# Performance work log

Hardware: AMD Instinct MI355X
Metric: run time of the kernel (lower is better)

Reference implementation:

```python
import jax, jax.numpy as jnp
import numpy as np
from jax import lax

B, NPG = 128, 1024          # graphs, nodes per graph
N = B * NPG                  # total nodes
AVG_DEG = 8
E = N * AVG_DEG              # total edges
F_N, F_E = 128, 32           # node / edge feature dims
LATENT = [32, 32, 32, 1]
D = sum(LATENT)              # total_latent_dim = 97
K = 30                       # sort-pooling k
C1, C2, KW2 = 16, 32, 5      # conv1d channels / kernel
OUT = 2
DENSE = ((K - 2) // 2 + 1 - KW2 + 1) * C2  # 352


def setup_inputs() -> dict:
    key = jax.random.key(0)
    ks = jax.random.split(key, 12)
    inp = {}
    inp["node_feat"] = jax.random.normal(ks[0], (N, F_N), jnp.float32)
    inp["edge_feat"] = jax.random.normal(ks[1], (E, F_E), jnp.float32)
    inp["edge_index"] = jax.random.randint(ks[2], (2, E), 0, N)
    dims = [F_N + F_E] + LATENT
    for i in range(4):
        inp[f"W{i}"] = jax.random.normal(ks[3 + i], (dims[i], dims[i + 1]), jnp.float32) * 0.05
        inp[f"b{i}"] = jnp.zeros((dims[i + 1],), jnp.float32)
    inp["w_conv1"] = jax.random.normal(ks[7], (C1, 1, D), jnp.float32) * 0.05
    inp["b_conv1"] = jnp.zeros((C1,), jnp.float32)
    inp["w_conv2"] = jax.random.normal(ks[8], (C2, C1, KW2), jnp.float32) * 0.05
    inp["b_conv2"] = jnp.zeros((C2,), jnp.float32)
    inp["w_out"] = jax.random.normal(ks[9], (DENSE, OUT), jnp.float32) * 0.05
    inp["b_out"] = jnp.zeros((OUT,), jnp.float32)
    return inp


def _maxpool2(x):
    # MaxPool1d(2, 2) over last axis of [B, C, L]
    return lax.reduce_window(x, -jnp.inf, lax.max, (1, 1, 2), (1, 1, 2), "VALID")


def _forward(node_feat, edge_feat, W0, b0, W1, b1, W2, b2, W3, b3,
             w_conv1, b_conv1, w_conv2, b_conv2, w_out, b_out, edge_index):
    src, dst = edge_index[0], edge_index[1]
    # degree with self-loop, as in DGCNN (divide by deg after linear)
    deg = jnp.ones((N,), node_feat.dtype).at[dst].add(1.0)
    # e2npool: sum incident edge features onto destination nodes
    e2n = jax.ops.segment_sum(edge_feat, dst, num_segments=N)
    cur = jnp.concatenate([node_feat, e2n], axis=1)  # [N, F_N+F_E]
    hops = []
    for W, b in ((W0, b0), (W1, b1), (W2, b2), (W3, b3)):
        # (A + I) X  -> Linear -> / deg -> tanh
        pooled = jax.ops.segment_sum(cur[src], dst, num_segments=N) + cur
        cur = jnp.tanh((pooled @ W + b) / deg[:, None])
        hops.append(cur)
    feat = jnp.concatenate(hops, axis=1).reshape(B, NPG, D)  # [B, NPG, 97]
    # SortPooling: top-k nodes per graph by last latent channel
    _, idx = lax.top_k(feat[:, :, -1], K)                    # [B, K]
    sp = jnp.take_along_axis(feat, idx[:, :, None], axis=1)  # [B, K, D]
    x = sp.reshape(B, 1, K * D)
    x = lax.conv_general_dilated(x, w_conv1, (D,), "VALID",
                                 dimension_numbers=("NCH", "OIH", "NCH"))
    x = jax.nn.relu(x + b_conv1[None, :, None])  # [B, 16, 30]
    x = _maxpool2(x)                              # [B, 16, 15]
    x = lax.conv_general_dilated(x, w_conv2, (1,), "VALID",
                                 dimension_numbers=("NCH", "OIH", "NCH"))
    x = jax.nn.relu(x + b_conv2[None, :, None])  # [B, 32, 11]
    x = x.reshape(B, -1)                          # [B, 352]
    return jax.nn.relu(x @ w_out + b_out)         # [B, OUT]


def reference(node_feat, edge_feat, edge_index, W0, b0, W1, b1, W2, b2, W3, b3,
              w_conv1, b_conv1, w_conv2, b_conv2, w_out, b_out):
    return _forward(node_feat, edge_feat, W0, b0, W1, b1, W2, b2, W3, b3,
                    w_conv1, b_conv1, w_conv2, b_conv2, w_out, b_out, edge_index)
```

## Files before the change

kernel.cpp:

```cpp
#include <hip/hip_runtime.h>
#include <hip/hip_bf16.h>
#include <math.h>

#define N_NODES 131072
#define N_EDGES 1048576
#define B_GR    128
#define NPG_    1024
#define KTOP    30


__global__ __launch_bounds__(256) void k_zero(int* cnt) {
    int i = blockIdx.x * 256 + threadIdx.x;
    if (i < N_NODES) cnt[i] = 0;
}

__global__ __launch_bounds__(256) void k_count(const int* __restrict__ dst, int* __restrict__ cnt) {
    int e = blockIdx.x * 256 + threadIdx.x;
    if (e < N_EDGES) atomicAdd(&cnt[dst[e]], 1);
}

__global__ __launch_bounds__(256) void k_scan1(const int* __restrict__ cnt,
                                               int* __restrict__ row_start,
                                               int* __restrict__ blocksum) {
    __shared__ int s[256];
    int t = threadIdx.x;
    int i = blockIdx.x * 256 + t;
    int v = cnt[i];
    s[t] = v; __syncthreads();
    for (int o = 1; o < 256; o <<= 1) {
        int x = (t >= o) ? s[t - o] : 0;
        __syncthreads();
        s[t] += x;
        __syncthreads();
    }
    row_start[i] = s[t] - v;
    if (t == 255) blocksum[blockIdx.x] = s[t];
}

__global__ __launch_bounds__(512) void k_scan2(int* __restrict__ blocksum) {
    __shared__ int s[512];
    int t = threadIdx.x;
    int v = blocksum[t];
    s[t] = v; __syncthreads();
    for (int o = 1; o < 512; o <<= 1) {
        int x = (t >= o) ? s[t - o] : 0;
        __syncthreads();
        s[t] += x;
        __syncthreads();
    }
    blocksum[t] = s[t] - v;
}

__global__ __launch_bounds__(256) void k_scan3(int* __restrict__ row_start,
                                               const int* __restrict__ blocksum,
                                               int* __restrict__ cursor) {
    int i = blockIdx.x * 256 + threadIdx.x;
    int r = row_start[i] + blocksum[blockIdx.x];
    row_start[i] = r;
    cursor[i] = r;
}

__global__ __launch_bounds__(256) void k_fill(const int* __restrict__ src,
                                              const int* __restrict__ dst,
                                              int* __restrict__ cursor,
                                              int2* __restrict__ csr) {
    int e = blockIdx.x * 256 + threadIdx.x;
    if (e < N_EDGES) {
        int d = dst[e];
        int pos = atomicAdd(&cursor[d], 1);
        csr[pos] = make_int2(src[e], e);
    }
}


__global__ __launch_bounds__(256) void k_esum(const float* __restrict__ ef,
                                              const int* __restrict__ row_start,
                                              const int* __restrict__ cnt,
                                              const int2* __restrict__ csr,
                                              float* __restrict__ esum) {
    int g = threadIdx.x >> 5, j = threadIdx.x & 31;
    int n = blockIdx.x * 8 + g;
    int start = row_start[n], len = cnt[n];
    const int2* ce = csr + start;
    float s = 0.f;
    int i = 0;
    for (; i + 8 <= len; i += 8) {
        int e0 = ce[i].y, e1 = ce[i + 1].y, e2 = ce[i + 2].y, e3 = ce[i + 3].y;
        int e4 = ce[i + 4].y, e5 = ce[i + 5].y, e6 = ce[i + 6].y, e7 = ce[i + 7].y;
        float a0 = ef[(size_t)e0 * 32 + j], a1 = ef[(size_t)e1 * 32 + j];
        float a2 = ef[(size_t)e2 * 32 + j], a3 = ef[(size_t)e3 * 32 + j];
        float a4 = ef[(size_t)e4 * 32 + j], a5 = ef[(size_t)e5 * 32 + j];
        float a6 = ef[(size_t)e6 * 32 + j], a7 = ef[(size_t)e7 * 32 + j];
        s += ((a0 + a1) + (a2 + a3)) + ((a4 + a5) + (a6 + a7));
    }
    for (; i < len; ++i) s += ef[(size_t)ce[i].y * 32 + j];
    esum[(size_t)n * 32 + j] = s;
}


__global__ __launch_bounds__(256) void k_gemm160(const float* __restrict__ nf,
                                                 const float* __restrict__ esum,
                                                 const float* __restrict__ W0,
                                                 float* __restrict__ z0) {
    __shared__ float a[64 * 161];
    int tid = threadIdx.x;
    int n0 = blockIdx.x * 64;
    const float* nfb = nf + (size_t)n0 * 128;
    for (int f = tid; f < 8192; f += 256) {
        int n = f >> 7, k = f & 127;
        a[n * 161 + k] = nfb[f];
    }
    const float* esb = esum + (size_t)n0 * 32;
    for (int f = tid; f < 2048; f += 256) {
        int n = f >> 5, k = f & 31;
        a[n * 161 + 128 + k] = esb[f];
    }
    __syncthreads();
    int wv = __builtin_amdgcn_readfirstlane(tid >> 6);
    int lane = tid & 63;
    int c0 = wv * 8;
    float acc[8] = {0.f, 0.f, 0.f, 0.f, 0.f, 0.f, 0.f, 0.f};
    const float* ar = a + lane * 161;
    for (int k = 0; k < 160; ++k) {
        float av = ar[k];
        #pragma unroll
        for (int jj = 0; jj < 8; ++jj)
            acc[jj] += av * W0[k * 32 + c0 + jj];
    }
    float* zr = z0 + (size_t)(n0 + lane) * 32 + c0;
    *(float4*)zr = make_float4(acc[0], acc[1], acc[2], acc[3]);
    *(float4*)(zr + 4) = make_float4(acc[4], acc[5], acc[6], acc[7]);
}


__global__ __launch_bounds__(256) void k_gemm32(const float* __restrict__ h,
                                                const float* __restrict__ W,
                                                float* __restrict__ zout) {
    __shared__ float a[64 * 33];
    int tid = threadIdx.x;
    int n0 = blockIdx.x * 64;
    const float* hb = h + (size_t)n0 * 32;
    for (int f = tid; f < 2048; f += 256) {
        int n = f >> 5, k = f & 31;
        a[n * 33 + k] = hb[f];
    }
    __syncthreads();
    int wv = __builtin_amdgcn_readfirstlane(tid >> 6);
    int lane = tid & 63;
    int c0 = wv * 8;
    float acc[8] = {0.f, 0.f, 0.f, 0.f, 0.f, 0.f, 0.f, 0.f};
    const float* ar = a + lane * 33;
    #pragma unroll
    for (int k = 0; k < 32; ++k) {
        float av = ar[k];
        #pragma unroll
        for (int jj = 0; jj < 8; ++jj)
            acc[jj] += av * W[k * 32 + c0 + jj];
    }
    float* zr = zout + (size_t)(n0 + lane) * 32 + c0;
    *(float4*)zr = make_float4(acc[0], acc[1], acc[2], acc[3]);
    *(float4*)(zr + 4) = make_float4(acc[4], acc[5], acc[6], acc[7]);
}


__global__ __launch_bounds__(256) void k_g(const float* __restrict__ zin,
                                           const int* __restrict__ row_start,
                                           const int* __restrict__ cnt,
                                           const int2* __restrict__ csr,
                                           const float* __restrict__ bias,
                                           float* __restrict__ hout) {
    int g = threadIdx.x >> 5, j = threadIdx.x & 31;
    int n = blockIdx.x * 8 + g;
    int start = row_start[n], len = cnt[n];
    const int2* cs = csr + start;
    float p = zin[(size_t)n * 32 + j];
    int i = 0;
    for (; i + 8 <= len; i += 8) {
        int s0 = cs[i].x, s1 = cs[i + 1].x, s2 = cs[i + 2].x, s3 = cs[i + 3].x;
        int s4 = cs[i + 4].x, s5 = cs[i + 5].x, s6 = cs[i + 6].x, s7 = cs[i + 7].x;
        float a0 = zin[(size_t)s0 * 32 + j], a1 = zin[(size_t)s1 * 32 + j];
        float a2 = zin[(size_t)s2 * 32 + j], a3 = zin[(size_t)s3 * 32 + j];
        float a4 = zin[(size_t)s4 * 32 + j], a5 = zin[(size_t)s5 * 32 + j];
        float a6 = zin[(size_t)s6 * 32 + j], a7 = zin[(size_t)s7 * 32 + j];
        p += ((a0 + a1) + (a2 + a3)) + ((a4 + a5) + (a6 + a7));
    }
    for (; i < len; ++i) p += zin[(size_t)cs[i].x * 32 + j];
    float deg = 1.f + (float)len;
    hout[(size_t)n * 32 + j] = tanhf((p + bias[j]) / deg);
}


__global__ __launch_bounds__(256) void k_g2(const float* __restrict__ zin,
                                            const int* __restrict__ row_start,
                                            const int* __restrict__ cnt,
                                            const int2* __restrict__ csr,
                                            const float* __restrict__ bias,
                                            const float* __restrict__ W3,
                                            float* __restrict__ hout,
                                            float* __restrict__ z3) {
    int g = threadIdx.x >> 5, j = threadIdx.x & 31;
    int n = blockIdx.x * 8 + g;
    int start = row_start[n], len = cnt[n];
    const int2* cs = csr + start;
    float p = zin[(size_t)n * 32 + j];
    int i = 0;
    for (; i + 8 <= len; i += 8) {
        int s0 = cs[i].x, s1 = cs[i + 1].x, s2 = cs[i + 2].x, s3 = cs[i + 3].x;
        int s4 = cs[i + 4].x, s5 = cs[i + 5].x, s6 = cs[i + 6].x, s7 = cs[i + 7].x;
        float a0 = zin[(size_t)s0 * 32 + j], a1 = zin[(size_t)s1 * 32 + j];
        float a2 = zin[(size_t)s2 * 32 + j], a3 = zin[(size_t)s3 * 32 + j];
        float a4 = zin[(size_t)s4 * 32 + j], a5 = zin[(size_t)s5 * 32 + j];
        float a6 = zin[(size_t)s6 * 32 + j], a7 = zin[(size_t)s7 * 32 + j];
        p += ((a0 + a1) + (a2 + a3)) + ((a4 + a5) + (a6 + a7));
    }
    for (; i < len; ++i) p += zin[(size_t)cs[i].x * 32 + j];
    float deg = 1.f + (float)len;
    float h = tanhf((p + bias[j]) / deg);
    hout[(size_t)n * 32 + j] = h;
    float t = h * W3[j];
    #pragma unroll
    for (int o = 16; o; o >>= 1) t += __shfl_xor(t, o, 32);
    if (j == 0) z3[n] = t;
}


__global__ __launch_bounds__(256) void k_g3(const float* __restrict__ z3,
                                            const int* __restrict__ row_start,
                                            const int* __restrict__ cnt,
                                            const int2* __restrict__ csr,
                                            const float* __restrict__ b3,
                                            float* __restrict__ val) {
    int n = blockIdx.x * 256 + threadIdx.x;
    int start = row_start[n], len = cnt[n];
    const int2* cs = csr + start;
    float s = z3[n];
    int i = 0;
    for (; i + 4 <= len; i += 4)
        s += z3[cs[i].x] + z3[cs[i + 1].x] + z3[cs[i + 2].x] + z3[cs[i + 3].x];
    for (; i < len; ++i) s += z3[cs[i].x];
    float deg = 1.f + (float)len;
    val[n] = tanhf((s + b3[0]) / deg);
}


__global__ __launch_bounds__(256) void k_head(const float* __restrict__ h0,
                                              const float* __restrict__ h1,
                                              const float* __restrict__ h2,
                                              const float* __restrict__ val,
                                              const float* __restrict__ wc1,
                                              const float* __restrict__ bc1,
                                              const float* __restrict__ wc2,
                                              const float* __restrict__ bc2,
                                              const float* __restrict__ wout,
                                              const float* __restrict__ bout,
                                              float* __restrict__ out) {
    __shared__ float vals[1024];
    __shared__ int selidx[KTOP];
    __shared__ float sp[KTOP * 97];
    __shared__ float y1[16 * 30];
    __shared__ float pool[16 * 15];
    __shared__ float y2[352];
    int b = blockIdx.x, tid = threadIdx.x;
    const float* vb = val + (size_t)b * NPG_;
    for (int u = tid; u < NPG_; u += 256) vals[u] = vb[u];
    __syncthreads();
    if (tid < 64) {
        unsigned long long keys[16];
        #pragma unroll
        for (int r = 0; r < 16; ++r) {
            int u = tid * 16 + r;
            unsigned int bb = __float_as_uint(vals[u]);
            unsigned int ord = (bb & 0x80000000u) ? ~bb : (bb | 0x80000000u);
            keys[r] = ((unsigned long long)ord << 32) |
                      (unsigned long long)(0xFFFFFFFFu - (unsigned int)u);
        }
        for (int k = 0; k < KTOP; ++k) {
            unsigned long long m = keys[0];
            #pragma unroll
            for (int r = 1; r < 16; ++r) m = (keys[r] > m) ? keys[r] : m;
            #pragma unroll
            for (int o = 32; o; o >>= 1) {
                unsigned long long t = __shfl_xor(m, o);
                m = (t > m) ? t : m;
            }
            int u = (int)(0xFFFFFFFFu - (unsigned int)(m & 0xFFFFFFFFull));
            if (tid == 0) selidx[k] = u;
            #pragma unroll
            for (int r = 0; r < 16; ++r)
                if (tid * 16 + r == u) keys[r] = 0ull;
        }
    }
    __syncthreads();
    size_t nb = (size_t)b * NPG_;
    for (int idx = tid; idx < KTOP * 32; idx += 256) {
        int t = idx >> 5, d = idx & 31;
        size_t s = (nb + (size_t)selidx[t]) * 32;
        sp[t * 97 + d]      = h0[s + d];
        sp[t * 97 + 32 + d] = h1[s + d];
        sp[t * 97 + 64 + d] = h2[s + d];
    }
    if (tid < KTOP) sp[tid * 97 + 96] = vb[selidx[tid]];
    __syncthreads();
    for (int idx = tid; idx < 480; idx += 256) {
        int t = idx >> 4, c = idx & 15;
        float acc = bc1[c];
        for (int d = 0; d < 97; ++d) acc += sp[t * 97 + d] * wc1[c * 97 + d];
        y1[c * 30 + t] = fmaxf(acc, 0.f);
    }
    __syncthreads();
    for (int idx = tid; idx < 240; idx += 256) {
        int c = idx / 15, u = idx - c * 15;
        pool[c * 15 + u] = fmaxf(y1[c * 30 + 2 * u], y1[c * 30 + 2 * u + 1]);
    }
    __syncthreads();
    for (int idx = tid; idx < 352; idx += 256) {
        int o = idx / 11, t = idx - o * 11;
        float acc = bc2[o];
        for (int i = 0; i < 16; ++i)
            for (int kk = 0; kk < 5; ++kk)
                acc += pool[i * 15 + t + kk] * wc2[(o * 16 + i) * 5 + kk];
        y2[idx] = fmaxf(acc, 0.f);
    }
    __syncthreads();
    if (tid < 2) {
        float acc = bout[tid];
        for (int m = 0; m < 352; ++m) acc += y2[m] * wout[m * 2 + tid];
        out[b * 2 + tid] = fmaxf(acc, 0.f);
    }
}


extern "C" void kernel_launch(void* const* d_in, const int* in_sizes, int n_in,
                              void* d_out, int out_size, void* d_ws, size_t ws_size,
                              hipStream_t stream) {
    const float* node_feat = (const float*)d_in[0];
    const float* edge_feat = (const float*)d_in[1];
    const int*   eidx      = (const int*)d_in[2];
    const float* W0 = (const float*)d_in[3];
    const float* b0 = (const float*)d_in[4];
    const float* W1 = (const float*)d_in[5];
    const float* b1 = (const float*)d_in[6];
    const float* W2 = (const float*)d_in[7];
    const float* b2 = (const float*)d_in[8];
    const float* W3 = (const float*)d_in[9];
    const float* b3 = (const float*)d_in[10];
    const float* wc1 = (const float*)d_in[11];
    const float* bc1 = (const float*)d_in[12];
    const float* wc2 = (const float*)d_in[13];
    const float* bc2 = (const float*)d_in[14];
    const float* wout = (const float*)d_in[15];
    const float* bout = (const float*)d_in[16];
    float* out = (float*)d_out;

    const int* src = eidx;
    const int* dst = eidx + N_EDGES;

    char* ws = (char*)d_ws;
    size_t off = 0;
    auto alloc = [&](size_t bytes) -> char* {
        char* p = ws + off;
        off += (bytes + 255) & ~(size_t)255;
        return p;
    };
    int* cnt       = (int*)alloc((size_t)N_NODES * 4);
    int* row_start = (int*)alloc((size_t)N_NODES * 4);
    int* cursor    = (int*)alloc((size_t)N_NODES * 4);
    int* blocksum  = (int*)alloc(512 * 4);
    int2* csr      = (int2*)alloc((size_t)N_EDGES * 8);
    float* esum    = (float*)alloc((size_t)N_NODES * 32 * 4);
    float* z0      = (float*)alloc((size_t)N_NODES * 32 * 4);
    float* z1      = (float*)alloc((size_t)N_NODES * 32 * 4);
    float* z2      = (float*)alloc((size_t)N_NODES * 32 * 4);
    float* h0      = (float*)alloc((size_t)N_NODES * 32 * 4);
    float* h1      = (float*)alloc((size_t)N_NODES * 32 * 4);
    float* h2      = (float*)alloc((size_t)N_NODES * 32 * 4);
    float* z3      = (float*)alloc((size_t)N_NODES * 4);
    float* val     = (float*)alloc((size_t)N_NODES * 4);
    (void)ws_size;

    k_zero<<<N_NODES / 256, 256, 0, stream>>>(cnt);
    k_count<<<N_EDGES / 256, 256, 0, stream>>>(dst, cnt);
    k_scan1<<<N_NODES / 256, 256, 0, stream>>>(cnt, row_start, blocksum);
    k_scan2<<<1, 512, 0, stream>>>(blocksum);
    k_scan3<<<N_NODES / 256, 256, 0, stream>>>(row_start, blocksum, cursor);
    k_fill<<<N_EDGES / 256, 256, 0, stream>>>(src, dst, cursor, csr);
    k_esum<<<N_NODES / 8, 256, 0, stream>>>(edge_feat, row_start, cnt, csr, esum);
    k_gemm160<<<N_NODES / 64, 256, 0, stream>>>(node_feat, esum, W0, z0);
    k_g<<<N_NODES / 8, 256, 0, stream>>>(z0, row_start, cnt, csr, b0, h0);
    k_gemm32<<<N_NODES / 64, 256, 0, stream>>>(h0, W1, z1);
    k_g<<<N_NODES / 8, 256, 0, stream>>>(z1, row_start, cnt, csr, b1, h1);
    k_gemm32<<<N_NODES / 64, 256, 0, stream>>>(h1, W2, z2);
    k_g2<<<N_NODES / 8, 256, 0, stream>>>(z2, row_start, cnt, csr, b2, W3, h2, z3);
    k_g3<<<N_NODES / 256, 256, 0, stream>>>(z3, row_start, cnt, csr, b3, val);
    k_head<<<B_GR, 256, 0, stream>>>(h0, h1, h2, val, wc1, bc1, wc2, bc2, wout, bout, out);
}
```

Baseline: 671.1 us.

## Fuse neighbor aggregation with following dense layer GEMMs

Merges the edge-feature sum into the first 160-wide GEMM kernel and each node-aggregation+tanh pass into the next layer's 32-wide GEMM, writing results straight into shared memory. This drops three kernel launches and the esum buffer plus the re-reading of h0/h1 from global memory. It also swaps the zero kernel for hipMemsetAsync. The cost is that each block now handles 64 nodes with 8 sequential gathers per 32-lane group, so there are fewer blocks and less parallelism for latency hiding during the irregular gathers.

```diff
diff --git a/kernel.cpp b/kernel.cpp
--- a/kernel.cpp
+++ b/kernel.cpp
@@ -8,11 +8,6 @@
 #define NPG_    1024
 #define KTOP    30
 
-
-__global__ __launch_bounds__(256) void k_zero(int* cnt) {
-    int i = blockIdx.x * 256 + threadIdx.x;
-    if (i < N_NODES) cnt[i] = 0;
-}
 
 __global__ __launch_bounds__(256) void k_count(const int* __restrict__ dst, int* __restrict__ cnt) {
     int e = blockIdx.x * 256 + threadIdx.x;
@@ -73,33 +68,11 @@
 }
 
 
-__global__ __launch_bounds__(256) void k_esum(const float* __restrict__ ef,
-                                              const int* __restrict__ row_start,
-                                              const int* __restrict__ cnt,
-                                              const int2* __restrict__ csr,
-                                              float* __restrict__ esum) {
-    int g = threadIdx.x >> 5, j = threadIdx.x & 31;
-    int n = blockIdx.x * 8 + g;
-    int start = row_start[n], len = cnt[n];
-    const int2* ce = csr + start;
-    float s = 0.f;
-    int i = 0;
-    for (; i + 8 <= len; i += 8) {
-        int e0 = ce[i].y, e1 = ce[i + 1].y, e2 = ce[i + 2].y, e3 = ce[i + 3].y;
-        int e4 = ce[i + 4].y, e5 = ce[i + 5].y, e6 = ce[i + 6].y, e7 = ce[i + 7].y;
-        float a0 = ef[(size_t)e0 * 32 + j], a1 = ef[(size_t)e1 * 32 + j];
-        float a2 = ef[(size_t)e2 * 32 + j], a3 = ef[(size_t)e3 * 32 + j];
-        float a4 = ef[(size_t)e4 * 32 + j], a5 = ef[(size_t)e5 * 32 + j];
-        float a6 = ef[(size_t)e6 * 32 + j], a7 = ef[(size_t)e7 * 32 + j];
-        s += ((a0 + a1) + (a2 + a3)) + ((a4 + a5) + (a6 + a7));
-    }
-    for (; i < len; ++i) s += ef[(size_t)ce[i].y * 32 + j];
-    esum[(size_t)n * 32 + j] = s;
-}
-
-
-__global__ __launch_bounds__(256) void k_gemm160(const float* __restrict__ nf,
-                                                 const float* __restrict__ esum,
+__global__ __launch_bounds__(256) void k_z0fused(const float* __restrict__ nf,
+                                                 const float* __restrict__ ef,
+                                                 const int* __restrict__ row_start,
+                                                 const int* __restrict__ cnt,
+                                                 const int2* __restrict__ csr,
                                                  const float* __restrict__ W0,
                                                  float* __restrict__ z0) {
     __shared__ float a[64 * 161];
@@ -107,13 +80,28 @@
     int n0 = blockIdx.x * 64;
     const float* nfb = nf + (size_t)n0 * 128;
     for (int f = tid; f < 8192; f += 256) {
-        int n = f >> 7, k = f & 127;
-        a[n * 161 + k] = nfb[f];
-    }
-    const float* esb = esum + (size_t)n0 * 32;
-    for (int f = tid; f < 2048; f += 256) {
-        int n = f >> 5, k = f & 31;
-        a[n * 161 + 128 + k] = esb[f];
+        int nl = f >> 7, k = f & 127;
+        a[nl * 161 + k] = nfb[f];
+    }
+    int g = tid >> 5, j = tid & 31;
+    for (int q = 0; q < 8; ++q) {
+        int nl = g * 8 + q;
+        int n = n0 + nl;
+        int start = row_start[n], len = cnt[n];
+        const int2* ce = csr + start;
+        float s = 0.f;
+        int i = 0;
+        for (; i + 8 <= len; i += 8) {
+            int e0 = ce[i].y, e1 = ce[i + 1].y, e2 = ce[i + 2].y, e3 = ce[i + 3].y;
+            int e4 = ce[i + 4].y, e5 = ce[i + 5].y, e6 = ce[i + 6].y, e7 = ce[i + 7].y;
+            float a0 = ef[(size_t)e0 * 32 + j], a1 = ef[(size_t)e1 * 32 + j];
+            float a2 = ef[(size_t)e2 * 32 + j], a3 = ef[(size_t)e3 * 32 + j];
+            float a4 = ef[(size_t)e4 * 32 + j], a5 = ef[(size_t)e5 * 32 + j];
+            float a6 = ef[(size_t)e6 * 32 + j], a7 = ef[(size_t)e7 * 32 + j];
+            s += ((a0 + a1) + (a2 + a3)) + ((a4 + a5) + (a6 + a7));
+        }
+        for (; i < len; ++i) s += ef[(size_t)ce[i].y * 32 + j];
+        a[nl * 161 + 128 + j] = s;
     }
     __syncthreads();
     int wv = __builtin_amdgcn_readfirstlane(tid >> 6);
@@ -133,16 +121,40 @@
 }
 
 
-__global__ __launch_bounds__(256) void k_gemm32(const float* __restrict__ h,
-                                                const float* __restrict__ W,
+__global__ __launch_bounds__(256) void k_gfused(const float* __restrict__ zin,
+                                                const int* __restrict__ row_start,
+                                                const int* __restrict__ cnt,
+                                                const int2* __restrict__ csr,
+                                                const float* __restrict__ bias,
+                                                const float* __restrict__ Wnext,
+                                                float* __restrict__ hout,
                                                 float* __restrict__ zout) {
     __shared__ float a[64 * 33];
     int tid = threadIdx.x;
     int n0 = blockIdx.x * 64;
-    const float* hb = h + (size_t)n0 * 32;
-    for (int f = tid; f < 2048; f += 256) {
-        int n = f >> 5, k = f & 31;
-        a[n * 33 + k] = hb[f];
+    int g = tid >> 5, j = tid & 31;
+    float bj = bias[j];
+    for (int q = 0; q < 8; ++q) {
+        int nl = g * 8 + q;
+        int n = n0 + nl;
+        int start = row_start[n], len = cnt[n];
+        const int2* cs = csr + start;
+        float p = zin[(size_t)n * 32 + j];
+        int i = 0;
+        for (; i + 8 <= len; i += 8) {
+            int s0 = cs[i].x, s1 = cs[i + 1].x, s2 = cs[i + 2].x, s3 = cs[i + 3].x;
+            int s4 = cs[i + 4].x, s5 = cs[i + 5].x, s6 = cs[i + 6].x, s7 = cs[i + 7].x;
+            float a0 = zin[(size_t)s0 * 32 + j], a1 = zin[(size_t)s1 * 32 + j];
+            float a2 = zin[(size_t)s2 * 32 + j], a3 = zin[(size_t)s3 * 32 + j];
+            float a4 = zin[(size_t)s4 * 32 + j], a5 = zin[(size_t)s5 * 32 + j];
+            float a6 = zin[(size_t)s6 * 32 + j], a7 = zin[(size_t)s7 * 32 + j];
+            p += ((a0 + a1) + (a2 + a3)) + ((a4 + a5) + (a6 + a7));
+        }
+        for (; i < len; ++i) p += zin[(size_t)cs[i].x * 32 + j];
+        float deg = 1.f + (float)len;
+        float h = tanhf((p + bj) / deg);
+        hout[(size_t)n * 32 + j] = h;
+        a[nl * 33 + j] = h;
     }
     __syncthreads();
     int wv = __builtin_amdgcn_readfirstlane(tid >> 6);
@@ -155,38 +167,11 @@
         float av = ar[k];
         #pragma unroll
         for (int jj = 0; jj < 8; ++jj)
-            acc[jj] += av * W[k * 32 + c0 + jj];
+            acc[jj] += av * Wnext[k * 32 + c0 + jj];
     }
     float* zr = zout + (size_t)(n0 + lane) * 32 + c0;
     *(float4*)zr = make_float4(acc[0], acc[1], acc[2], acc[3]);
     *(float4*)(zr + 4) = make_float4(acc[4], acc[5], acc[6], acc[7]);
-}
-
-
-__global__ __launch_bounds__(256) void k_g(const float* __restrict__ zin,
-                                           const int* __restrict__ row_start,
-                                           const int* __restrict__ cnt,
-                                           const int2* __restrict__ csr,
-                                           const float* __restrict__ bias,
-                                           float* __restrict__ hout) {
-    int g = threadIdx.x >> 5, j = threadIdx.x & 31;
-    int n = blockIdx.x * 8 + g;
-    int start = row_start[n], len = cnt[n];
-    const int2* cs = csr + start;
-    float p = zin[(size_t)n * 32 + j];
-    int i = 0;
-    for (; i + 8 <= len; i += 8) {
-        int s0 = cs[i].x, s1 = cs[i + 1].x, s2 = cs[i + 2].x, s3 = cs[i + 3].x;
-        int s4 = cs[i + 4].x, s5 = cs[i + 5].x, s6 = cs[i + 6].x, s7 = cs[i + 7].x;
-        float a0 = zin[(size_t)s0 * 32 + j], a1 = zin[(size_t)s1 * 32 + j];
-        float a2 = zin[(size_t)s2 * 32 + j], a3 = zin[(size_t)s3 * 32 + j];
-        float a4 = zin[(size_t)s4 * 32 + j], a5 = zin[(size_t)s5 * 32 + j];
-        float a6 = zin[(size_t)s6 * 32 + j], a7 = zin[(size_t)s7 * 32 + j];
-        p += ((a0 + a1) + (a2 + a3)) + ((a4 + a5) + (a6 + a7));
-    }
-    for (; i < len; ++i) p += zin[(size_t)cs[i].x * 32 + j];
-    float deg = 1.f + (float)len;
-    hout[(size_t)n * 32 + j] = tanhf((p + bias[j]) / deg);
 }
 
 
@@ -367,7 +352,6 @@
     int* cursor    = (int*)alloc((size_t)N_NODES * 4);
     int* blocksum  = (int*)alloc(512 * 4);
     int2* csr      = (int2*)alloc((size_t)N_EDGES * 8);
-    float* esum    = (float*)alloc((size_t)N_NODES * 32 * 4);
     float* z0      = (float*)alloc((size_t)N_NODES * 32 * 4);
     float* z1      = (float*)alloc((size_t)N_NODES * 32 * 4);
     float* z2      = (float*)alloc((size_t)N_NODES * 32 * 4);
@@ -378,18 +362,15 @@
     float* val     = (float*)alloc((size_t)N_NODES * 4);
     (void)ws_size;
 
-    k_zero<<<N_NODES / 256, 256, 0, stream>>>(cnt);
+    hipMemsetAsync(cnt, 0, (size_t)N_NODES * 4, stream);
     k_count<<<N_EDGES / 256, 256, 0, stream>>>(dst, cnt);
     k_scan1<<<N_NODES / 256, 256, 0, stream>>>(cnt, row_start, blocksum);
     k_scan2<<<1, 512, 0, stream>>>(blocksum);
     k_scan3<<<N_NODES / 256, 256, 0, stream>>>(row_start, blocksum, cursor);
     k_fill<<<N_EDGES / 256, 256, 0, stream>>>(src, dst, cursor, csr);
-    k_esum<<<N_NODES / 8, 256, 0, stream>>>(edge_feat, row_start, cnt, csr, esum);
-    k_gemm160<<<N_NODES / 64, 256, 0, stream>>>(node_feat, esum, W0, z0);
-    k_g<<<N_NODES / 8, 256, 0, stream>>>(z0, row_start, cnt, csr, b0, h0);
-    k_gemm32<<<N_NODES / 64, 256, 0, stream>>>(h0, W1, z1);
-    k_g<<<N_NODES / 8, 256, 0, stream>>>(z1, row_start, cnt, csr, b1, h1);
-    k_gemm32<<<N_NODES / 64, 256, 0, stream>>>(h1, W2, z2);
+    k_z0fused<<<N_NODES / 64, 256, 0, stream>>>(node_feat, edge_feat, row_start, cnt, csr, W0, z0);
+    k_gfused<<<N_NODES / 64, 256, 0, stream>>>(z0, row_start, cnt, csr, b0, W1, h0, z1);
+    k_gfused<<<N_NODES / 64, 256, 0, stream>>>(z1, row_start, cnt, csr, b1, W2, h1, z2);
     k_g2<<<N_NODES / 8, 256, 0, stream>>>(z2, row_start, cnt, csr, b2, W3, h2, z3);
     k_g3<<<N_NODES / 256, 256, 0, stream>>>(z3, row_start, cnt, csr, b3, val);
     k_head<<<B_GR, 256, 0, stream>>>(h0, h1, h2, val, wc1, bc1, wc2, bc2, wout, bout, out);
```

After: 740.6 us. 1.1x slower.
